# Kernel optimization log

Hardware: AMD Instinct MI355X
Metric: run time of the kernel (lower is better)

## Reference

```python
import jax, jax.numpy as jnp
import numpy as np

N_NODES = 100000

def setup_inputs() -> dict:
    key = jax.random.key(0)
    k = jax.random.split(key, 6)
    N, E, D = N_NODES, 1600000, 128
    x = jax.random.normal(k[0], (N, D), dtype=jnp.float32)
    edge_src = jax.random.randint(k[1], (E,), 0, N, dtype=jnp.int32)
    edge_dst = jax.random.randint(k[2], (E,), 0, N, dtype=jnp.int32)
    edge_weight = jax.random.uniform(k[3], (E,), dtype=jnp.float32)
    W1 = jax.random.normal(k[4], (D, D), dtype=jnp.float32) * (1.0 / np.sqrt(D))
    W2 = jax.random.normal(k[5], (D, D), dtype=jnp.float32) * (1.0 / np.sqrt(D))
    return {"x": x, "edge_src": edge_src, "edge_dst": edge_dst,
            "edge_weight": edge_weight, "W1": W1, "W2": W2}

def _graph_conv(x, W, src, dst, ew, n_nodes):
    # GraphConv: h = A @ (x @ W); A given as weighted edge list.
    h = x @ W                               # [N, D_out]
    msg = h[src] * ew[:, None]              # [E, D_out] gather + scale
    return jax.ops.segment_sum(msg, dst, num_segments=n_nodes)  # [N, D_out]

def reference(x, edge_src, edge_dst, edge_weight, W1, W2):
    n = x.shape[0]
    # layer 1: tanh(GraphConv) ; Dropout(0) is identity
    x = jnp.tanh(_graph_conv(x, W1, edge_src, edge_dst, edge_weight, n))
    # layer 2
    x = jnp.tanh(_graph_conv(x, W2, edge_src, edge_dst, edge_weight, n))
    return x
```

## Files before the change

kernel.cpp:

```cpp
#include <hip/hip_runtime.h>
#include <hip/hip_bf16.h>

#define N_NODES 100000
#define N_EDGES 1600000
#define D 128
#define BSZ 128
#define NBUCK 782
#define EPW 8192
#define NWG1 ((N_EDGES + EPW - 1) / EPW)
#define CAP 4096
#define OTS 272

typedef unsigned int  uint4n  __attribute__((ext_vector_type(4)));
typedef float         float4n __attribute__((ext_vector_type(4)));
typedef _Float16      half8n  __attribute__((ext_vector_type(8)));
typedef _Float16      half4n  __attribute__((ext_vector_type(4)));

#define SWZ(row, kb) (((row) << 8) + ((kb) ^ (((row) & 15) << 4)))

__device__ __forceinline__ float fast_tanh(float x) {
    float t = __builtin_amdgcn_exp2f(x * 2.885390081777927f);
    return 1.0f - 2.0f * __builtin_amdgcn_rcpf(t + 1.0f);
}

__global__ __launch_bounds__(256) void k_wprep(const float* __restrict__ W1,
                                               const float* __restrict__ W2,
                                               char* __restrict__ Wt,
                                               int* __restrict__ bcnt) {
    if (blockIdx.x == 32) {
        for (int i = threadIdx.x; i < NBUCK; i += 256) bcnt[i] = 0;
        return;
    }
    const float* W = (blockIdx.x < 16) ? W1 : W2;
    char* dst = Wt + ((blockIdx.x < 16) ? 0 : 32768);
    int t = (blockIdx.x & 15) * 256 + threadIdx.x;
    int idx = t * 4;
    int k = idx >> 7, c = idx & 127;
    float4 wv = *(const float4*)&W[idx];
    *(_Float16*)(dst + SWZ(c + 0, k * 2)) = (_Float16)wv.x;
    *(_Float16*)(dst + SWZ(c + 1, k * 2)) = (_Float16)wv.y;
    *(_Float16*)(dst + SWZ(c + 2, k * 2)) = (_Float16)wv.z;
    *(_Float16*)(dst + SWZ(c + 3, k * 2)) = (_Float16)wv.w;
}


__global__ __launch_bounds__(256) void k_hist1(const int* __restrict__ dst,
                                               int* __restrict__ bcnt) {
    __shared__ int h[NBUCK];
    for (int i = threadIdx.x; i < NBUCK; i += 256) h[i] = 0;
    __syncthreads();
    int base = blockIdx.x * EPW;
    int end  = min(base + EPW, N_EDGES);
    for (int i = base + threadIdx.x; i < end; i += 256)
        atomicAdd(&h[dst[i] >> 7], 1);
    __syncthreads();
    for (int i = threadIdx.x; i < NBUCK; i += 256)
        if (h[i]) atomicAdd(&bcnt[i], h[i]);
}

__global__ void k_scanN(const int* __restrict__ bcnt, int* __restrict__ boff,
                        int* __restrict__ gcur) {
    __shared__ int tmp[256];
    int tid = threadIdx.x;
    int carry = 0;
    for (int c = 0; c < (NBUCK + 255) / 256; c++) {
        int i = c * 256 + tid;
        int v = (i < NBUCK) ? bcnt[i] : 0;
        tmp[tid] = v;
        __syncthreads();
        int run = v;
        for (int off = 1; off < 256; off <<= 1) {
            int t = (tid >= off) ? tmp[tid - off] : 0;
            __syncthreads();
            run += t;
            tmp[tid] = run;
            __syncthreads();
        }
        int excl = carry + run - v;
        if (i < NBUCK) { boff[i] = excl; gcur[i] = excl; }
        int tot = tmp[255];
        __syncthreads();
        carry += tot;
    }
    if (tid == 0) boff[NBUCK] = N_EDGES;
}

__global__ __launch_bounds__(256) void k_scat1(const int* __restrict__ src,
                                               const int* __restrict__ dst,
                                               const float* __restrict__ ew,
                                               int* __restrict__ gcur,
                                               int2* __restrict__ ebuf) {
    __shared__ int h[NBUCK];
    __shared__ int rb[NBUCK];
    for (int i = threadIdx.x; i < NBUCK; i += 256) h[i] = 0;
    __syncthreads();
    int base = blockIdx.x * EPW;
    int end  = min(base + EPW, N_EDGES);
    for (int i = base + threadIdx.x; i < end; i += 256)
        atomicAdd(&h[dst[i] >> 7], 1);
    __syncthreads();
    for (int i = threadIdx.x; i < NBUCK; i += 256) {
        int c = h[i];
        if (c) rb[i] = atomicAdd(&gcur[i], c);
    }
    __syncthreads();
    for (int i = base + threadIdx.x; i < end; i += 256) {
        int d  = dst[i];
        int bk = d >> 7;
        int p  = atomicAdd(&rb[bk], 1);
        ebuf[p] = make_int2((src[i] << 8) | (d & 127), __float_as_int(ew[i]));
    }
}

__global__ __launch_bounds__(512) void k_sortb(int2* __restrict__ ebuf,
                                               const int* __restrict__ boff,
                                               int* __restrict__ rowptr) {
    __shared__ int2 se[CAP];
    __shared__ int cnt[BSZ];
    __shared__ int cur[BSZ];
    int tid = threadIdx.x;
    int b   = blockIdx.x;
    int e0 = boff[b], e1 = boff[b + 1];
    int m  = e1 - e0;
    if (tid < BSZ) cnt[tid] = 0;
    __syncthreads();
    int2 ovf;
    bool hasOvf = false;
    for (int i = tid; i < m; i += 512) {
        int2 v = ebuf[e0 + i];
        if (i < CAP) se[i] = v;
        else { ovf = v; hasOvf = true; }
        atomicAdd(&cnt[v.x & (BSZ - 1)], 1);
    }
    __syncthreads();
    if (tid < 64) {
        int a  = cnt[tid * 2], bq = cnt[tid * 2 + 1];
        int s  = a + bq;
        int incl = s;
        #pragma unroll
        for (int off = 1; off < 64; off <<= 1) {
            int t = __shfl_up(incl, off, 64);
            if (tid >= off) incl += t;
        }
        int ex = incl - s;
        cur[tid * 2]     = ex;
        cur[tid * 2 + 1] = ex + a;
        int node = b * BSZ + tid * 2;
        if (node     <= N_NODES) rowptr[node]     = e0 + ex;
        if (node + 1 <= N_NODES) rowptr[node + 1] = e0 + ex + a;
    }
    __syncthreads();
    for (int i = tid; i < m && i < CAP; i += 512) {
        int2 v = se[i];
        int p = atomicAdd(&cur[v.x & (BSZ - 1)], 1);
        ebuf[e0 + p] = v;
    }
    if (hasOvf) {
        int p = atomicAdd(&cur[ovf.x & (BSZ - 1)], 1);
        ebuf[e0 + p] = ovf;
    }
}

template<bool XF16>
__global__ __launch_bounds__(256) void k_gemm(const void* __restrict__ Xv,
                                              const char* __restrict__ Wt,
                                              _Float16* __restrict__ H, int n) {
    __shared__ char smem[17408];
    char* sA = smem;
    int tid  = threadIdx.x;
    int lane = tid & 63, w = tid >> 6;
    int rows0 = blockIdx.x * 64;

    int rb = (w >> 1) * 32;
    int cb = (w & 1) * 64;
    int lr = lane & 15;
    int kg = (lane >> 4) * 16;

    if (XF16) {
        const _Float16* Xh = (const _Float16*)Xv;
        #pragma unroll
        for (int rep = 0; rep < 4; rep++) {
            int ef = rep * 2048 + tid * 8;
            int r = ef >> 7, c = ef & 127;
            int rg = rows0 + r;
            half8n v = half8n(0);
            if (rg < n) v = *(const half8n*)(Xh + (size_t)rg * 128 + c);
            *(half8n*)(sA + SWZ(r, c * 2)) = v;
        }
    } else {
        const float* Xf = (const float*)Xv;
        #pragma unroll
        for (int rep = 0; rep < 8; rep++) {
            int ef = rep * 1024 + tid * 4;
            int r = ef >> 7, c = ef & 127;
            int rg = rows0 + r;
            float4 xv = make_float4(0.f, 0.f, 0.f, 0.f);
            if (rg < n) xv = *(const float4*)(Xf + (size_t)rg * 128 + c);
            half4n hv;
            hv[0] = (_Float16)xv.x; hv[1] = (_Float16)xv.y;
            hv[2] = (_Float16)xv.z; hv[3] = (_Float16)xv.w;
            *(half4n*)(sA + SWZ(r, c * 2)) = hv;
        }
    }
    __syncthreads();

    float4n acc[2][4] = {};
    #pragma unroll
    for (int ks = 0; ks < 4; ks++) {
        half8n bwk[4];
        #pragma unroll
        for (int ct = 0; ct < 4; ct++)
            bwk[ct] = *(const half8n*)(Wt + SWZ(cb + ct * 16 + lr, ks * 64 + kg));
        half8n af[2];
        #pragma unroll
        for (int rt = 0; rt < 2; rt++)
            af[rt] = *(const half8n*)(sA + SWZ(rb + rt * 16 + lr, ks * 64 + kg));
        #pragma unroll
        for (int rt = 0; rt < 2; rt++)
            #pragma unroll
            for (int ct = 0; ct < 4; ct++)
                acc[rt][ct] = __builtin_amdgcn_mfma_f32_16x16x32_f16(af[rt], bwk[ct], acc[rt][ct], 0, 0, 0);
    }

    __syncthreads();
    char* OT = smem;
    int rloc = rb + (lane >> 4) * 4;
    #pragma unroll
    for (int rt = 0; rt < 2; rt++) {
        #pragma unroll
        for (int ct = 0; ct < 4; ct++) {
            int col = cb + ct * 16 + lr;
            #pragma unroll
            for (int r = 0; r < 4; r++)
                *(_Float16*)(OT + (rloc + rt * 16 + r) * OTS + col * 2) = (_Float16)acc[rt][ct][r];
        }
    }
    __syncthreads();
    #pragma unroll
    for (int rep = 0; rep < 4; rep++) {
        int ef = rep * 2048 + tid * 8;
        int r = ef >> 7, c = ef & 127;
        int rg = rows0 + r;
        if (rg < n) {
            half8n v = *(const half8n*)(OT + r * OTS + c * 2);
            *(half8n*)&H[(size_t)rg * 128 + c] = v;
        }
    }
}

template<bool OUTF16>
__global__ __launch_bounds__(256) void k_agg(const _Float16* __restrict__ H,
                                             const int* __restrict__ rowptr,
                                             const int2* __restrict__ ebuf,
                                             void* __restrict__ outv, int n) {
    int wid  = (blockIdx.x * 256 + threadIdx.x) >> 6;
    int lane = threadIdx.x & 63;
    if (wid >= n) return;
    int g = lane >> 4;
    int c = lane & 15;
    const char* Hc = (const char*)H + (c << 4);
    int e0 = rowptr[wid], e1 = rowptr[wid + 1];
    int m  = e1 - e0;
    int nfull = m >> 2;
    float acc[8] = {};
    const int2* ep = ebuf + e0 + g;
    #pragma unroll 2
    for (int it = 0; it < nfull; ++it, ep += 4) {
        int2 ed = *ep;
        float w = __int_as_float(ed.y);
        half8n v = *(const half8n*)(Hc + (size_t)((unsigned)ed.x & 0xFFFFFF00u));
        #pragma unroll
        for (int j = 0; j < 8; j++) acc[j] = __builtin_fmaf((float)v[j], w, acc[j]);
    }
    if (m & 3) {
        int e  = e0 + nfull * 4 + g;
        int ec = (e < e1) ? e : (e1 - 1);
        int2 ed = ebuf[ec];
        float w = (e < e1) ? __int_as_float(ed.y) : 0.f;
        half8n v = *(const half8n*)(Hc + (size_t)((unsigned)ed.x & 0xFFFFFF00u));
        #pragma unroll
        for (int j = 0; j < 8; j++) acc[j] = __builtin_fmaf((float)v[j], w, acc[j]);
    }
    float t[8];
    #pragma unroll
    for (int j = 0; j < 8; j++) {
        float a = acc[j];
        a += __shfl_xor(a, 16, 64);
        a += __shfl_xor(a, 32, 64);
        t[j] = fast_tanh(a);
    }
    if (OUTF16) {
        if (g == 0) {
            half8n hv;
            #pragma unroll
            for (int j = 0; j < 8; j++) hv[j] = (_Float16)t[j];
            uint4n o = *(uint4n*)&hv;
            __builtin_nontemporal_store(o, (uint4n*)((_Float16*)outv + (size_t)wid * 128 + c * 8));
        }
    } else {
        if (g < 2) {
            float4n o;
            o.x = t[g * 4 + 0]; o.y = t[g * 4 + 1];
            o.z = t[g * 4 + 2]; o.w = t[g * 4 + 3];
            __builtin_nontemporal_store(o, (float4n*)((float*)outv + (size_t)wid * 128 + c * 8 + g * 4));
        }
    }
}


extern "C" void kernel_launch(void* const* d_in, const int* in_sizes, int n_in,
                              void* d_out, int out_size, void* d_ws, size_t ws_size,
                              hipStream_t stream) {
    const float* x    = (const float*)d_in[0];
    const int*   esrc = (const int*)d_in[1];
    const int*   edst = (const int*)d_in[2];
    const float* ew   = (const float*)d_in[3];
    const float* W1   = (const float*)d_in[4];
    const float* W2   = (const float*)d_in[5];
    float* out = (float*)d_out;

    _Float16* hbuf = (_Float16*)d_ws;
    _Float16* act1 = hbuf + (size_t)N_NODES * D;
    int2* ebuf     = (int2*)(act1 + (size_t)N_NODES * D);
    int*  bcnt     = (int*)(ebuf + N_EDGES);
    int*  boff     = bcnt + NBUCK;
    int*  gcur     = boff + (NBUCK + 1);
    int*  rowptr   = gcur + NBUCK;
    char* Wt       = (char*)(rowptr + N_NODES + 8);
    (void)ws_size; (void)in_sizes; (void)n_in; (void)out_size;

    k_wprep<<<33, 256, 0, stream>>>(W1, W2, Wt, bcnt);
    k_hist1<<<NWG1, 256, 0, stream>>>(edst, bcnt);
    k_scanN<<<1, 256, 0, stream>>>(bcnt, boff, gcur);
    k_scat1<<<NWG1, 256, 0, stream>>>(esrc, edst, ew, gcur, ebuf);
    k_sortb<<<NBUCK, 512, 0, stream>>>(ebuf, boff, rowptr);

    int gemm_blocks = (N_NODES + 63) / 64;
    int agg_blocks  = (N_NODES * 64 + 255) / 256;

    k_gemm<false><<<gemm_blocks, 256, 0, stream>>>(x, Wt, hbuf, N_NODES);
    k_agg<true><<<agg_blocks, 256, 0, stream>>>(hbuf, rowptr, ebuf, act1, N_NODES);
    k_gemm<true><<<gemm_blocks, 256, 0, stream>>>(act1, Wt + 32768, hbuf, N_NODES);
    k_agg<false><<<agg_blocks, 256, 0, stream>>>(hbuf, rowptr, ebuf, out, N_NODES);
}
```

Before: 231.9 us.

## Map one node per 16-lane group in aggregation instead of one per wavefront

The aggregation kernel now gives each node to a 16-lane group rather than a full 64-lane wavefront, so a wavefront handles four nodes and each group walks that node's edge list serially, two edges per iteration. This drops the cross-group shuffle reduction, lets every lane take part in the output stores, and cuts the launch to a quarter as many blocks. The trade-off is divergence: group lanes in the same wavefront now run loops of different lengths depending on node degree, and there is less edge-level parallelism per node.

```diff
diff --git a/kernel.cpp b/kernel.cpp
--- a/kernel.cpp
+++ b/kernel.cpp
@@ -253,57 +253,50 @@
                                              const int* __restrict__ rowptr,
                                              const int2* __restrict__ ebuf,
                                              void* __restrict__ outv, int n) {
-    int wid  = (blockIdx.x * 256 + threadIdx.x) >> 6;
+    int wv   = (blockIdx.x * 256 + threadIdx.x) >> 6;
     int lane = threadIdx.x & 63;
-    if (wid >= n) return;
     int g = lane >> 4;
     int c = lane & 15;
+    int node = wv * 4 + g;
+    if (node >= n) return;
     const char* Hc = (const char*)H + (c << 4);
-    int e0 = rowptr[wid], e1 = rowptr[wid + 1];
-    int m  = e1 - e0;
-    int nfull = m >> 2;
+    int e0 = rowptr[node], e1 = rowptr[node + 1];
     float acc[8] = {};
-    const int2* ep = ebuf + e0 + g;
-    #pragma unroll 2
-    for (int it = 0; it < nfull; ++it, ep += 4) {
-        int2 ed = *ep;
+    int e = e0;
+    for (; e + 2 <= e1; e += 2) {
+        int2 eda = ebuf[e];
+        int2 edb = ebuf[e + 1];
+        half8n va = *(const half8n*)(Hc + (size_t)((unsigned)eda.x & 0xFFFFFF00u));
+        half8n vb = *(const half8n*)(Hc + (size_t)((unsigned)edb.x & 0xFFFFFF00u));
+        float wa = __int_as_float(eda.y);
+        float wb = __int_as_float(edb.y);
+        #pragma unroll
+        for (int j = 0; j < 8; j++) acc[j] = __builtin_fmaf((float)va[j], wa, acc[j]);
+        #pragma unroll
+        for (int j = 0; j < 8; j++) acc[j] = __builtin_fmaf((float)vb[j], wb, acc[j]);
+    }
+    if (e < e1) {
+        int2 ed = ebuf[e];
+        half8n v = *(const half8n*)(Hc + (size_t)((unsigned)ed.x & 0xFFFFFF00u));
         float w = __int_as_float(ed.y);
-        half8n v = *(const half8n*)(Hc + (size_t)((unsigned)ed.x & 0xFFFFFF00u));
         #pragma unroll
         for (int j = 0; j < 8; j++) acc[j] = __builtin_fmaf((float)v[j], w, acc[j]);
     }
-    if (m & 3) {
-        int e  = e0 + nfull * 4 + g;
-        int ec = (e < e1) ? e : (e1 - 1);
-        int2 ed = ebuf[ec];
-        float w = (e < e1) ? __int_as_float(ed.y) : 0.f;
-        half8n v = *(const half8n*)(Hc + (size_t)((unsigned)ed.x & 0xFFFFFF00u));
-        #pragma unroll
-        for (int j = 0; j < 8; j++) acc[j] = __builtin_fmaf((float)v[j], w, acc[j]);
-    }
-    float t[8];
-    #pragma unroll
-    for (int j = 0; j < 8; j++) {
-        float a = acc[j];
-        a += __shfl_xor(a, 16, 64);
-        a += __shfl_xor(a, 32, 64);
-        t[j] = fast_tanh(a);
-    }
     if (OUTF16) {
-        if (g == 0) {
-            half8n hv;
-            #pragma unroll
-            for (int j = 0; j < 8; j++) hv[j] = (_Float16)t[j];
-            uint4n o = *(uint4n*)&hv;
-            __builtin_nontemporal_store(o, (uint4n*)((_Float16*)outv + (size_t)wid * 128 + c * 8));
-        }
+        half8n hv;
+        #pragma unroll
+        for (int j = 0; j < 8; j++) hv[j] = (_Float16)fast_tanh(acc[j]);
+        __builtin_nontemporal_store(*(uint4n*)&hv,
+            (uint4n*)((_Float16*)outv + (size_t)node * 128 + c * 8));
     } else {
-        if (g < 2) {
-            float4n o;
-            o.x = t[g * 4 + 0]; o.y = t[g * 4 + 1];
-            o.z = t[g * 4 + 2]; o.w = t[g * 4 + 3];
-            __builtin_nontemporal_store(o, (float4n*)((float*)outv + (size_t)wid * 128 + c * 8 + g * 4));
-        }
+        float* op = (float*)outv + (size_t)node * 128 + c * 8;
+        float4n o0, o1;
+        o0.x = fast_tanh(acc[0]); o0.y = fast_tanh(acc[1]);
+        o0.z = fast_tanh(acc[2]); o0.w = fast_tanh(acc[3]);
+        o1.x = fast_tanh(acc[4]); o1.y = fast_tanh(acc[5]);
+        o1.z = fast_tanh(acc[6]); o1.w = fast_tanh(acc[7]);
+        __builtin_nontemporal_store(o0, (float4n*)op);
+        __builtin_nontemporal_store(o1, (float4n*)(op + 4));
     }
 }
 
@@ -336,7 +329,7 @@
     k_sortb<<<NBUCK, 512, 0, stream>>>(ebuf, boff, rowptr);
 
     int gemm_blocks = (N_NODES + 63) / 64;
-    int agg_blocks  = (N_NODES * 64 + 255) / 256;
+    int agg_blocks  = (N_NODES + 15) / 16;
 
     k_gemm<false><<<gemm_blocks, 256, 0, stream>>>(x, Wt, hbuf, N_NODES);
     k_agg<true><<<agg_blocks, 256, 0, stream>>>(hbuf, rowptr, ebuf, act1, N_NODES);
```

After: 232.8 us. Within noise of the previous version (+0.4%).
